# Performance work log

Measured on AMD Instinct MI355X. Metric: run time of the kernel, lower is better.

Reference implementation:

```python
import jax, jax.numpy as jnp
import numpy as np
from jax import lax


def conv2d(x, w, b, stride, pad):
    # x: NCHW, w: OIHW (PyTorch Conv2d layout)
    y = lax.conv_general_dilated(x, w, (stride, stride), ((pad, pad), (pad, pad)),
                                 dimension_numbers=('NCHW', 'OIHW', 'NCHW'))
    return y + b[None, :, None, None]


def conv_transpose2d(x, w, b, stride, pad):
    # PyTorch ConvTranspose2d weight layout: (in_ch, out_ch, kH, kW).
    # Equivalent to a conv with lhs dilation, flipped kernel, in/out swapped.
    k = w.shape[2]
    w2 = jnp.transpose(jnp.flip(w, (2, 3)), (1, 0, 2, 3))  # (out, in, k, k)
    p = k - 1 - pad
    y = lax.conv_general_dilated(x, w2, (1, 1), ((p, p), (p, p)),
                                 lhs_dilation=(stride, stride),
                                 dimension_numbers=('NCHW', 'OIHW', 'NCHW'))
    return y + b[None, :, None, None]


def setup_inputs() -> dict:
    key = jax.random.key(0)
    ks = jax.random.split(key, 8)
    K, D = 512, 64  # num_embeddings, embedding_dim
    x = jax.random.uniform(ks[0], (32, 3, 256, 256), jnp.float32)

    def he(k, shape, fan_in):
        return jax.random.normal(k, shape, jnp.float32) * np.float32(np.sqrt(2.0 / fan_in))

    w1 = he(ks[1], (64, 3, 4, 4), 3 * 16);   b1 = jnp.zeros((64,), jnp.float32)
    w2 = he(ks[2], (D, 64, 4, 4), 64 * 16);  b2 = jnp.zeros((D,), jnp.float32)
    # codebook init: uniform(-1/K, 1/K) as in the torch module
    codebook = jax.random.uniform(ks[3], (K, D), jnp.float32, -1.0 / K, 1.0 / K)
    dw1 = he(ks[4], (D, 64, 4, 4), D * 16);  db1 = jnp.zeros((64,), jnp.float32)
    dw2 = he(ks[5], (64, 3, 4, 4), 64 * 16); db2 = jnp.zeros((3,), jnp.float32)
    return dict(x=x, w1=w1, b1=b1, w2=w2, b2=b2, codebook=codebook,
                dw1=dw1, db1=db1, dw2=dw2, db2=db2)


def reference(x, w1, b1, w2, b2, codebook, dw1, db1, dw2, db2):
    # Encoder
    z_e = jax.nn.relu(conv2d(x, w1, b1, 2, 1))
    z_e = jax.nn.relu(conv2d(z_e, w2, b2, 2, 1))  # (N, D, H/4, W/4)
    D = z_e.shape[1]
    # Faithful to torch: .view(-1, C) on contiguous NCHW (NO channel permute)
    zf = z_e.reshape(-1, D)  # (N*Hq*Wq, D) given D == Hq here numerically; rows are contiguous slices
    # ||z - e||^2 = ||z||^2 + ||e||^2 - 2 z.e  -> (M, K) distance matrix
    d = (jnp.sum(zf * zf, axis=1, keepdims=True)
         + jnp.sum(codebook * codebook, axis=1)
         - 2.0 * (zf @ codebook.T))
    idx = jnp.argmin(d, axis=1)           # (M,) int
    z_q = codebook[idx].reshape(z_e.shape)  # gather + reshape back to z_e shape
    # Decoder
    h = jax.nn.relu(conv_transpose2d(z_q, dw1, db1, 2, 1))
    x_recon = jax.nn.sigmoid(conv_transpose2d(h, dw2, db2, 2, 1))
    return x_recon, z_q
```

## Files before the change

kernel.cpp:

```cpp
#include <hip/hip_runtime.h>
#include <math.h>


typedef __attribute__((ext_vector_type(8))) short short8;
typedef __attribute__((ext_vector_type(4))) short short4v;
typedef __attribute__((ext_vector_type(4))) float f32x4;

#define MFMA16(a, b, c) __builtin_amdgcn_mfma_f32_16x16x32_bf16((a), (b), (c), 0, 0, 0)

__device__ __forceinline__ short f2bf(float f) {
  union { float f; unsigned u; } x; x.f = f;
  unsigned r = (x.u + 0x7FFFu + ((x.u >> 16) & 1u)) >> 16;
  return (short)r;
}
__device__ __forceinline__ float bf2f(short s) {
  union { unsigned u; float f; } x;
  x.u = ((unsigned)(unsigned short)s) << 16;
  return x.f;
}

__global__ __launch_bounds__(256) void k_prep(const float* __restrict__ w2,
                                              const float* __restrict__ dw1,
                                              const float* __restrict__ dw2,
                                              const float* __restrict__ cb,
                                              short* __restrict__ A2,
                                              short* __restrict__ AD1,
                                              short* __restrict__ AD2,
                                              short* __restrict__ cbb,
                                              float* __restrict__ cnm) {
  int i = blockIdx.x * 256 + threadIdx.x;
  {
    int t = i >> 12, oc = (i >> 6) & 63, c = i & 63;
    A2[i] = f2bf(w2[(oc * 64 + c) * 16 + t]);
  }
  {
    int p = i >> 14, ab = (i >> 12) & 3, oc = (i >> 6) & 63, c = i & 63;
    int kh = 1 - (p >> 1) + 2 * (ab >> 1);
    int kw = 1 - (p & 1) + 2 * (ab & 1);
    AD1[i] = f2bf(dw1[(c * 64 + oc) * 16 + kh * 4 + kw]);
  }
  if (i < 16384) {
    int p = i >> 12, ab = (i >> 10) & 3, oc = (i >> 6) & 15, c = i & 63;
    int kh = 1 - (p >> 1) + 2 * (ab >> 1);
    int kw = 1 - (p & 1) + 2 * (ab & 1);
    short v = 0;
    if (oc < 3) v = f2bf(dw2[(c * 3 + oc) * 16 + kh * 4 + kw]);
    AD2[i] = v;
  }
  if (i < 32768) cbb[i] = f2bf(cb[i]);
  if (i < 512) {
    float s = 0.f;
    for (int d = 0; d < 64; ++d) { float v = cb[i * 64 + d]; s += v * v; }
    cnm[i] = s;
  }
}

__global__ __launch_bounds__(256) void k_conv1(const float* __restrict__ x,
                                               const float* __restrict__ w1,
                                               const float* __restrict__ b1,
                                               short* __restrict__ z1T) {
  __shared__ float sW[3 * 16 * 64];
  __shared__ float sB[64];
  __shared__ float sIn[3 * 34 * 34];
  __shared__ short sOutC[256 * 72];
  const int tid = threadIdx.x;

  {
    float tw[12];
#pragma unroll
    for (int it = 0; it < 12; ++it) {
      int i = tid + 256 * it;
      int oc = i & 63, t = (i >> 6) & 15, c = i >> 10;
      tw[it] = w1[(oc * 3 + c) * 16 + t];
    }
#pragma unroll
    for (int it = 0; it < 12; ++it) sW[tid + 256 * it] = tw[it];
  }
  if (tid < 64) sB[tid] = b1[tid];

  const int b = blockIdx.x;
  const int n = b >> 6;
  const int tile = b & 63;
  const int tr = tile >> 3, tc = tile & 7;
  const int oh0 = tr * 16, ow0 = tc * 16;
  const int ih_base = oh0 * 2 - 1, iw_base = ow0 * 2 - 1;

  {
    float t[14]; bool vd[14];
#pragma unroll
    for (int it = 0; it < 14; ++it) {
      int i = tid + 256 * it;
      vd[it] = i < 3468;
      int ii = vd[it] ? i : 0;
      int c = ii / 1156;
      int rem = ii - c * 1156;
      int r = rem / 34;
      int col = rem - r * 34;
      int ih = ih_base + r, iw = iw_base + col;
      float v = 0.f;
      if (vd[it] && (unsigned)ih < 256u && (unsigned)iw < 256u)
        v = x[((n * 3 + c) * 256 + ih) * 256 + iw];
      t[it] = v;
    }
#pragma unroll
    for (int it = 0; it < 14; ++it)
      if (vd[it]) sIn[tid + 256 * it] = t[it];
  }
  __syncthreads();

  const int ty = tid >> 4, tx = tid & 15;
  float acc[64];
#pragma unroll
  for (int j = 0; j < 64; ++j) acc[j] = sB[j];

  for (int c = 0; c < 3; ++c) {
    for (int t = 0; t < 16; ++t) {
      int kh = t >> 2, kw = t & 3;
      float v = sIn[c * 1156 + (2 * ty + kh) * 34 + (2 * tx + kw)];
      const float4* wp = (const float4*)&sW[(c * 16 + t) * 64];
#pragma unroll
      for (int j = 0; j < 16; ++j) {
        float4 w4 = wp[j];
        acc[4 * j + 0] += v * w4.x;
        acc[4 * j + 1] += v * w4.y;
        acc[4 * j + 2] += v * w4.z;
        acc[4 * j + 3] += v * w4.w;
      }
    }
  }

  const int sp = ty * 16 + tx;
#pragma unroll
  for (int kk = 0; kk < 8; ++kk) {
    short8 v;
#pragma unroll
    for (int t2 = 0; t2 < 8; ++t2) {
      float r = acc[8 * kk + t2];
      v[t2] = f2bf(r > 0.f ? r : 0.f);
    }
    *(short8*)&sOutC[sp * 72 + 8 * kk] = v;
  }
  __syncthreads();
  const int r = tid >> 4, jj = tid & 15;
#pragma unroll
  for (int it = 0; it < 8; ++it) {
    int chunk = jj + 16 * it;
    int owL = chunk >> 3, c8 = chunk & 7;
    short8 v = *(const short8*)&sOutC[(r * 16 + owL) * 72 + 8 * c8];
    *(short8*)(z1T + (((long)(n * 128 + oh0 + r) * 128) + ow0 + owL) * 64 + 8 * c8) = v;
  }
}

__global__ __launch_bounds__(256) void k_conv2(const short* __restrict__ z1T,
                                               const short* __restrict__ A2,
                                               const float* __restrict__ b2,
                                               short* __restrict__ ze) {
  __shared__ char smemC[62400];
  __shared__ float sB2c[64];
  short* slab = (short*)smemC;
  short* sOut = (short*)smemC;

  const int tid = threadIdx.x;
  if (tid < 64) sB2c[tid] = b2[tid];
  const int b = blockIdx.x;
  const int n = b >> 5;
  const int oh0 = (b & 31) * 2;
  const int w = tid >> 6, l = tid & 63;
  const int row = w >> 1, mh = w & 1;
  const int e = l & 15, kg = l >> 4;
  const int ih0 = 2 * oh0 - 1;

  f32x4 acc[2][4];
#pragma unroll
  for (int mi = 0; mi < 2; ++mi)
#pragma unroll
    for (int nt = 0; nt < 4; ++nt) acc[mi][nt] = (f32x4){0.f, 0.f, 0.f, 0.f};

  for (int p = 0; p < 2; ++p) {
    const int c0 = 32 * p;
    __syncthreads();
    {
      short8 ta[7]; int off[7];
#pragma unroll
      for (int it = 0; it < 7; ++it) {
        int i = tid + 256 * it;
        int r = i / 520;
        int rem = i - r * 520;
        int iwL = rem >> 2, li = rem & 3;
        int ih = ih0 + r, iw = iwL - 1;
        off[it] = 8 * ((r * 130 + iwL) * 5 + li);
        short8 v = {0, 0, 0, 0, 0, 0, 0, 0};
        if ((unsigned)ih < 128u && (unsigned)iw < 128u)
          v = *(const short8*)(z1T + (((long)(n * 128 + ih) * 128) + iw) * 64 + c0 + 8 * li);
        ta[it] = v;
      }
#pragma unroll
      for (int it = 0; it < 7; ++it) *(short8*)&slab[off[it]] = ta[it];
    }
    {
      short8 tb[6]; int off[6]; bool vd[6];
#pragma unroll
      for (int it = 0; it < 6; ++it) {
        int i = tid + 256 * (7 + it);
        vd[it] = i < 3120;
        int ii = vd[it] ? i : 0;
        int r = ii / 520;
        int rem = ii - r * 520;
        int iwL = rem >> 2, li = rem & 3;
        int ih = ih0 + r, iw = iwL - 1;
        off[it] = 8 * ((r * 130 + iwL) * 5 + li);
        short8 v = {0, 0, 0, 0, 0, 0, 0, 0};
        if (vd[it] && (unsigned)ih < 128u && (unsigned)iw < 128u)
          v = *(const short8*)(z1T + (((long)(n * 128 + ih) * 128) + iw) * 64 + c0 + 8 * li);
        tb[it] = v;
      }
#pragma unroll
      for (int it = 0; it < 6; ++it)
        if (vd[it]) *(short8*)&slab[off[it]] = tb[it];
    }
    __syncthreads();

    for (int t = 0; t < 16; ++t) {
      const int kh = t >> 2, kw = t & 3;
      const int rL = 2 * row + kh;
      short8 aF[2], bF[4];
#pragma unroll
      for (int mi = 0; mi < 2; ++mi)
        aF[mi] = *(const short8*)(A2 + ((t * 64 + 32 * mh + 16 * mi + e) * 64) + c0 + 8 * kg);
#pragma unroll
      for (int nt = 0; nt < 4; ++nt) {
        int iwL = 2 * (nt * 16 + e) + kw;
        bF[nt] = *(const short8*)&slab[8 * ((rL * 130 + iwL) * 5 + kg)];
      }
#pragma unroll
      for (int mi = 0; mi < 2; ++mi)
#pragma unroll
        for (int nt = 0; nt < 4; ++nt)
          acc[mi][nt] = MFMA16(aF[mi], bF[nt], acc[mi][nt]);
    }
  }

  __syncthreads();
#pragma unroll
  for (int mi = 0; mi < 2; ++mi)
#pragma unroll
    for (int nt = 0; nt < 4; ++nt)
#pragma unroll
      for (int rr = 0; rr < 4; ++rr) {
        int oc = 32 * mh + 16 * mi + 4 * kg + rr;
        float v = acc[mi][nt][rr] + sB2c[oc];
        sOut[(row * 64 + oc) * 68 + nt * 16 + e] = f2bf(v > 0.f ? v : 0.f);
      }
  __syncthreads();
  {
    int oc = 32 * mh + (l >> 1);
    int half = l & 1;
#pragma unroll
    for (int j = 0; j < 8; ++j) {
      short4v v = *(const short4v*)&sOut[(row * 64 + oc) * 68 + 32 * half + 4 * j];
      *(short4v*)(ze + (((long)(n * 64 + oc) * 64) + oh0 + row) * 64 + 32 * half + 4 * j) = v;
    }
  }
}

__global__ __launch_bounds__(256) void k_vq(const short* __restrict__ zeb,
                                            const short* __restrict__ cbb,
                                            const float* __restrict__ cnm,
                                            const float* __restrict__ cb,
                                            float* __restrict__ zq,
                                            short* __restrict__ zqT) {
  __shared__ short sT[64 * 68];
  const int tid = threadIdx.x;
  const int wv = tid >> 6, l = tid & 63;
  const int e = l & 15, kg = l >> 4;
  const int b = blockIdx.x;
  const int n = b >> 6, h = b & 63;

  const short* zebase = zeb + (((long)(n * 64 + 16 * wv + e) * 64) + h) * 64;
  short8 aF0 = *(const short8*)(zebase + 8 * kg);
  short8 aF1 = *(const short8*)(zebase + 32 + 8 * kg);

  float bestD[4];
  int bestI[4];
#pragma unroll
  for (int rr = 0; rr < 4; ++rr) { bestD[rr] = 3.4e38f; bestI[rr] = 0; }

  for (int ch = 0; ch < 8; ++ch) {
    f32x4 acc[4];
#pragma unroll
    for (int nt = 0; nt < 4; ++nt) {
      acc[nt] = (f32x4){0.f, 0.f, 0.f, 0.f};
      const short* cbase = cbb + (ch * 64 + nt * 16 + e) * 64;
      short8 b0 = *(const short8*)(cbase + 8 * kg);
      short8 b1 = *(const short8*)(cbase + 32 + 8 * kg);
      acc[nt] = MFMA16(aF0, b0, acc[nt]);
      acc[nt] = MFMA16(aF1, b1, acc[nt]);
    }
#pragma unroll
    for (int nt = 0; nt < 4; ++nt) {
      int code = ch * 64 + nt * 16 + e;
      float cn = cnm[code];
#pragma unroll
      for (int rr = 0; rr < 4; ++rr) {
        float d = cn - 2.f * acc[nt][rr];
        if (d < bestD[rr]) { bestD[rr] = d; bestI[rr] = code; }
      }
    }
  }
#pragma unroll
  for (int m = 1; m <= 8; m <<= 1) {
#pragma unroll
    for (int rr = 0; rr < 4; ++rr) {
      float od = __shfl_xor(bestD[rr], m);
      int oi = __shfl_xor(bestI[rr], m);
      if (od < bestD[rr] || (od == bestD[rr] && oi < bestI[rr])) {
        bestD[rr] = od; bestI[rr] = oi;
      }
    }
  }
#pragma unroll
  for (int rr = 0; rr < 4; ++rr) {
    int c = 16 * wv + 4 * kg + rr;
    int idx = bestI[rr];
    float4 v = *(const float4*)(cb + idx * 64 + 4 * e);
    *(float4*)(zq + (((long)(n * 64 + c) * 64) + h) * 64 + 4 * e) = v;
    sT[(4 * e + 0) * 68 + c] = f2bf(v.x);
    sT[(4 * e + 1) * 68 + c] = f2bf(v.y);
    sT[(4 * e + 2) * 68 + c] = f2bf(v.z);
    sT[(4 * e + 3) * 68 + c] = f2bf(v.w);
  }
  __syncthreads();
  {
    int wq = tid >> 2, hq = tid & 3;
    short8 v0 = *(const short8*)&sT[wq * 68 + 16 * hq];
    short8 v1 = *(const short8*)&sT[wq * 68 + 16 * hq + 8];
    short* dst = zqT + (((long)(n * 64 + h) * 64) + wq) * 64 + 16 * hq;
    *(short8*)dst = v0;
    *(short8*)(dst + 8) = v1;
  }
}

__global__ __launch_bounds__(256) void k_deconv1(const short* __restrict__ zqT,
                                                 const short* __restrict__ AD1,
                                                 const float* __restrict__ db1,
                                                 short* __restrict__ hT) {
  __shared__ char smemD[34816];
  __shared__ float sBias[64];
  short* slab = (short*)smemD;
  short* sOut = (short*)smemD;

  const int tid = threadIdx.x;
  if (tid < 64) sBias[tid] = db1[tid];
  const int b = blockIdx.x;
  const int n = b >> 6, i0 = b & 63;
  const int w = tid >> 6, l = tid & 63;
  const int ph = w >> 1, pw = w & 1;
  const int e = l & 15, kg = l >> 4;

  {
    short8 t[7]; int off[7]; bool vd[7];
#pragma unroll
    for (int it = 0; it < 7; ++it) {
      int i = tid + 256 * it;
      vd[it] = i < 1584;
      int ii = vd[it] ? i : 0;
      int r = ii / 528;
      int rem = ii - r * 528;
      int iwL = rem >> 3, li = rem & 7;
      int ih = i0 - 1 + r, iw = iwL - 1;
      off[it] = (r * 66 + iwL) * 72 + 8 * li;
      short8 v = {0, 0, 0, 0, 0, 0, 0, 0};
      if (vd[it] && (unsigned)ih < 64u && (unsigned)iw < 64u)
        v = *(const short8*)(zqT + (((long)(n * 64 + ih) * 64) + iw) * 64 + 8 * li);
      t[it] = v;
    }
#pragma unroll
    for (int it = 0; it < 7; ++it)
      if (vd[it]) *(short8*)&slab[off[it]] = t[it];
  }
  __syncthreads();

  f32x4 acc[4][4];
#pragma unroll
  for (int m = 0; m < 4; ++m)
#pragma unroll
    for (int nt = 0; nt < 4; ++nt) acc[m][nt] = (f32x4){0.f, 0.f, 0.f, 0.f};

  for (int ab = 0; ab < 4; ++ab) {
    const int rL = 1 + ph - (ab >> 1);
    const int coff = pw - (ab & 1) + 1;
#pragma unroll
    for (int ks = 0; ks < 2; ++ks) {
      short8 aF[4], bF[4];
#pragma unroll
      for (int m = 0; m < 4; ++m)
        aF[m] = *(const short8*)(AD1 + (((w * 4 + ab) * 64 + 16 * m + e) * 64) + 32 * ks + 8 * kg);
#pragma unroll
      for (int nt = 0; nt < 4; ++nt) {
        int iwL = nt * 16 + e + coff;
        bF[nt] = *(const short8*)&slab[(rL * 66 + iwL) * 72 + 32 * ks + 8 * kg];
      }
#pragma unroll
      for (int m = 0; m < 4; ++m)
#pragma unroll
        for (int nt = 0; nt < 4; ++nt)
          acc[m][nt] = MFMA16(aF[m], bF[nt], acc[m][nt]);
    }
  }

  __syncthreads();
#pragma unroll
  for (int m = 0; m < 4; ++m)
#pragma unroll
    for (int nt = 0; nt < 4; ++nt) {
      int owIdx = nt * 16 + e;
      int oc0 = 16 * m + 4 * kg;
      short4v o;
#pragma unroll
      for (int rr = 0; rr < 4; ++rr) {
        float v = acc[m][nt][rr] + sBias[oc0 + rr];
        o[rr] = f2bf(v > 0.f ? v : 0.f);
      }
      *(short4v*)&sOut[((w * 64 + owIdx) * 68) + oc0] = o;
    }
  __syncthreads();
  {
    const int oh = 2 * i0 + ph;
    const int ow = 2 * l + pw;
    short* dst = hT + (((long)(n * 128 + oh) * 128) + ow) * 64;
#pragma unroll
    for (int j = 0; j < 16; ++j) {
      short4v v = *(const short4v*)&sOut[((w * 64 + l) * 68) + 4 * j];
      *(short4v*)(dst + 4 * j) = v;
    }
  }
}

__global__ __launch_bounds__(512) void k_deconv2(const short* __restrict__ hT,
                                                 const short* __restrict__ AD2,
                                                 const float* __restrict__ db2,
                                                 float* __restrict__ xr) {
  __shared__ __align__(16) char smem[56160];
  __shared__ float sB2[3];
  short* slab = (short*)smem;
  float* sOut = (float*)smem;

  const int tid = threadIdx.x;
  if (tid < 3) sB2[tid] = db2[tid];
  const int b = blockIdx.x;
  const int n = b >> 5;
  const int band = b & 31;
  const int w = tid >> 6, l = tid & 63;
  const int ph = w >> 2, pw = (w >> 1) & 1, chf = w & 1;
  const int p = ph * 2 + pw;
  const int e = l & 15, kg = l >> 4;

  int soff[7]; long sga[7]; bool sv[7], sinb[7];
#pragma unroll
  for (int it = 0; it < 7; ++it) {
    int i = tid + 512 * it;
    sv[it] = i < 3120;
    int ii = sv[it] ? i : 0;
    int r = ii / 520;
    int rm = ii - r * 520;
    int iwL = rm >> 2, li = rm & 3;
    int ih = 4 * band - 1 + r, iw = iwL - 1;
    sinb[it] = sv[it] && (unsigned)ih < 128u && (unsigned)iw < 128u;
    soff[it] = (r * 130 + iwL) * 36 + 8 * li;
    sga[it] = (((long)(n * 128 + ih) * 128) + iw) * 64 + 8 * li;
  }

  {
    short8 t0[7];
#pragma unroll
    for (int it = 0; it < 7; ++it) {
      short8 v = {0, 0, 0, 0, 0, 0, 0, 0};
      if (sinb[it]) v = *(const short8*)(hT + sga[it]);
      t0[it] = v;
    }
#pragma unroll
    for (int it = 0; it < 7; ++it)
      if (sv[it]) *(short8*)&slab[soff[it]] = t0[it];
  }
  __syncthreads();

  short8 t1[7];
#pragma unroll
  for (int it = 0; it < 7; ++it) {
    short8 v = {0, 0, 0, 0, 0, 0, 0, 0};
    if (sinb[it]) v = *(const short8*)(hT + sga[it] + 32);
    t1[it] = v;
  }

  f32x4 acc[4][4];
#pragma unroll
  for (int j = 0; j < 4; ++j)
#pragma unroll
    for (int nt = 0; nt < 4; ++nt) acc[j][nt] = (f32x4){0.f, 0.f, 0.f, 0.f};

  const int colBase = 64 * chf + e + pw + 1;
  {
    short8 aF[4];
#pragma unroll
    for (int ab = 0; ab < 4; ++ab)
      aF[ab] = *(const short8*)(AD2 + (((p * 4 + ab) * 16 + e) * 64) + 8 * kg);
#pragma unroll
    for (int ab = 0; ab < 4; ++ab) {
      const int a = ab >> 1, bb = ab & 1;
#pragma unroll
      for (int j = 0; j < 4; ++j) {
        const int rL = j + ph - a + 1;
#pragma unroll
        for (int nt = 0; nt < 4; ++nt) {
          const int iwL = nt * 16 + colBase - bb;
          short8 bf = *(const short8*)&slab[(rL * 130 + iwL) * 36 + 8 * kg];
          acc[j][nt] = MFMA16(aF[ab], bf, acc[j][nt]);
        }
      }
    }
  }
  __syncthreads();

#pragma unroll
  for (int it = 0; it < 7; ++it)
    if (sv[it]) *(short8*)&slab[soff[it]] = t1[it];
  __syncthreads();
  {
    short8 aF[4];
#pragma unroll
    for (int ab = 0; ab < 4; ++ab)
      aF[ab] = *(const short8*)(AD2 + (((p * 4 + ab) * 16 + e) * 64) + 32 + 8 * kg);
#pragma unroll
    for (int ab = 0; ab < 4; ++ab) {
      const int a = ab >> 1, bb = ab & 1;
#pragma unroll
      for (int j = 0; j < 4; ++j) {
        const int rL = j + ph - a + 1;
#pragma unroll
        for (int nt = 0; nt < 4; ++nt) {
          const int iwL = nt * 16 + colBase - bb;
          short8 bf = *(const short8*)&slab[(rL * 130 + iwL) * 36 + 8 * kg];
          acc[j][nt] = MFMA16(aF[ab], bf, acc[j][nt]);
        }
      }
    }
  }
  __syncthreads();

  if (kg == 0) {
#pragma unroll
    for (int j = 0; j < 4; ++j)
#pragma unroll
      for (int nt = 0; nt < 4; ++nt) {
        int ohl = 2 * j + ph;
        int ow = 2 * (64 * chf + nt * 16 + e) + pw;
#pragma unroll
        for (int rr = 0; rr < 3; ++rr) {
          float v = 1.f / (1.f + expf(-(acc[j][nt][rr] + sB2[rr])));
          sOut[(rr * 8 + ohl) * 256 + ow] = v;
        }
      }
  }
  __syncthreads();
#pragma unroll
  for (int it = 0; it < 3; ++it) {
    int i = tid + 512 * it;
    int oc = i / 512, rem = i - oc * 512;
    int ohl = rem >> 6, c4 = rem & 63;
    float4 v = ((const float4*)sOut)[i];
    *(float4*)(xr + (((long)(n * 3 + oc) * 256) + 8 * band + ohl) * 256 + 4 * c4) = v;
  }
}

extern "C" void kernel_launch(void* const* d_in, const int* in_sizes, int n_in,
                              void* d_out, int out_size, void* d_ws, size_t ws_size,
                              hipStream_t stream) {
  (void)in_sizes; (void)n_in; (void)out_size; (void)ws_size;

  const float* x   = (const float*)d_in[0];
  const float* w1  = (const float*)d_in[1];
  const float* b1  = (const float*)d_in[2];
  const float* w2  = (const float*)d_in[3];
  const float* b2  = (const float*)d_in[4];
  const float* cb  = (const float*)d_in[5];
  const float* dw1 = (const float*)d_in[6];
  const float* db1 = (const float*)d_in[7];
  const float* dw2 = (const float*)d_in[8];
  const float* db2 = (const float*)d_in[9];

  char* wsb = (char*)d_ws;
  short* z1T = (short*)wsb;
  short* zeb = (short*)(wsb + 67108864);
  short* zqT = (short*)(wsb + 83886080);
  short* A2  = (short*)(wsb + 100663296);
  short* AD1 = (short*)(wsb + 100794368);
  short* cbb = (short*)(wsb + 100925440);
  float* cnm = (float*)(wsb + 100990976);
  short* AD2 = (short*)(wsb + 100993024);
  short* hT  = z1T;

  float* xr = (float*)d_out;
  float* zq = (float*)d_out + 6291456;

  k_prep<<<256, 256, 0, stream>>>(w2, dw1, dw2, cb, A2, AD1, AD2, cbb, cnm);
  k_conv1<<<2048, 256, 0, stream>>>(x, w1, b1, z1T);
  k_conv2<<<1024, 256, 0, stream>>>(z1T, A2, b2, zeb);
  k_vq<<<2048, 256, 0, stream>>>(zeb, cbb, cnm, cb, zq, zqT);
  k_deconv1<<<2048, 256, 0, stream>>>(zqT, AD1, db1, hT);
  k_deconv2<<<1024, 512, 0, stream>>>(hT, AD2, db2, xr);
}
```

Baseline: 471.6 us.

## Load deconv input fragments directly from global instead of staging LDS slabs

Both transposed-conv kernels stop staging the input halo into shared memory. Each wave now loads its MFMA B fragments straight from global memory into registers. In deconv2 those loads rotate through two row buffers, interleaved with the MFMAs, and the bias is read directly from global. This removes the LDS staging barriers and shrinks shared memory, which could raise occupancy, but overlapping windows are now fetched redundantly from global/L2 and register pressure goes up.

After: 477.8 us. About the same (+1.3%).

```diff
diff --git a/kernel.cpp b/kernel.cpp
--- a/kernel.cpp
+++ b/kernel.cpp
@@ -344,85 +344,76 @@
                                                  const short* __restrict__ AD1,
                                                  const float* __restrict__ db1,
                                                  short* __restrict__ hT) {
-  __shared__ char smemD[34816];
-  __shared__ float sBias[64];
-  short* slab = (short*)smemD;
-  short* sOut = (short*)smemD;
-
+  __shared__ short sOut[4 * 64 * 68];
   const int tid = threadIdx.x;
-  if (tid < 64) sBias[tid] = db1[tid];
   const int b = blockIdx.x;
   const int n = b >> 6, i0 = b & 63;
   const int w = tid >> 6, l = tid & 63;
   const int ph = w >> 1, pw = w & 1;
   const int e = l & 15, kg = l >> 4;
 
-  {
-    short8 t[7]; int off[7]; bool vd[7];
-#pragma unroll
-    for (int it = 0; it < 7; ++it) {
-      int i = tid + 256 * it;
-      vd[it] = i < 1584;
-      int ii = vd[it] ? i : 0;
-      int r = ii / 528;
-      int rem = ii - r * 528;
-      int iwL = rem >> 3, li = rem & 7;
-      int ih = i0 - 1 + r, iw = iwL - 1;
-      off[it] = (r * 66 + iwL) * 72 + 8 * li;
-      short8 v = {0, 0, 0, 0, 0, 0, 0, 0};
-      if (vd[it] && (unsigned)ih < 64u && (unsigned)iw < 64u)
-        v = *(const short8*)(zqT + (((long)(n * 64 + ih) * 64) + iw) * 64 + 8 * li);
-      t[it] = v;
-    }
-#pragma unroll
-    for (int it = 0; it < 7; ++it)
-      if (vd[it]) *(short8*)&slab[off[it]] = t[it];
-  }
-  __syncthreads();
-
   f32x4 acc[4][4];
 #pragma unroll
   for (int m = 0; m < 4; ++m)
 #pragma unroll
     for (int nt = 0; nt < 4; ++nt) acc[m][nt] = (f32x4){0.f, 0.f, 0.f, 0.f};
 
-  for (int ab = 0; ab < 4; ++ab) {
-    const int rL = 1 + ph - (ab >> 1);
-    const int coff = pw - (ab & 1) + 1;
-#pragma unroll
-    for (int ks = 0; ks < 2; ++ks) {
-      short8 aF[4], bF[4];
-#pragma unroll
-      for (int m = 0; m < 4; ++m)
-        aF[m] = *(const short8*)(AD1 + (((w * 4 + ab) * 64 + 16 * m + e) * 64) + 32 * ks + 8 * kg);
+#pragma unroll
+  for (int a = 0; a < 2; ++a) {
+    const int ih = i0 + ph - a;
+    const bool rowOk = (unsigned)ih < 64u;
+    const short* rowp = zqT + ((long)(n * 64 + ih) * 64) * 64 + 8 * kg;
+
+    short8 Bf[2][2][4];
+#pragma unroll
+    for (int bb = 0; bb < 2; ++bb)
 #pragma unroll
       for (int nt = 0; nt < 4; ++nt) {
-        int iwL = nt * 16 + e + coff;
-        bF[nt] = *(const short8*)&slab[(rL * 66 + iwL) * 72 + 32 * ks + 8 * kg];
-      }
-#pragma unroll
-      for (int m = 0; m < 4; ++m)
-#pragma unroll
-        for (int nt = 0; nt < 4; ++nt)
-          acc[m][nt] = MFMA16(aF[m], bF[nt], acc[m][nt]);
-    }
-  }
-
-  __syncthreads();
-#pragma unroll
-  for (int m = 0; m < 4; ++m)
+        const int iw = nt * 16 + e + pw - bb;
+        const bool v = rowOk && ((unsigned)iw < 64u);
+#pragma unroll
+        for (int ks = 0; ks < 2; ++ks) {
+          short8 t = {0, 0, 0, 0, 0, 0, 0, 0};
+          if (v) t = *(const short8*)(rowp + (long)iw * 64 + 32 * ks);
+          Bf[bb][ks][nt] = t;
+        }
+      }
+
+#pragma unroll
+    for (int bb = 0; bb < 2; ++bb) {
+      const int ab = 2 * a + bb;
+#pragma unroll
+      for (int ks = 0; ks < 2; ++ks) {
+        short8 aF[4];
+#pragma unroll
+        for (int m = 0; m < 4; ++m)
+          aF[m] = *(const short8*)(AD1 + (((w * 4 + ab) * 64 + 16 * m + e) * 64) + 32 * ks + 8 * kg);
+#pragma unroll
+        for (int m = 0; m < 4; ++m)
+#pragma unroll
+          for (int nt = 0; nt < 4; ++nt)
+            acc[m][nt] = MFMA16(aF[m], Bf[bb][ks][nt], acc[m][nt]);
+      }
+    }
+  }
+
+#pragma unroll
+  for (int m = 0; m < 4; ++m) {
+    const int oc0 = 16 * m + 4 * kg;
+    const float4 bv = *(const float4*)(db1 + oc0);
+    const float bvv[4] = {bv.x, bv.y, bv.z, bv.w};
 #pragma unroll
     for (int nt = 0; nt < 4; ++nt) {
       int owIdx = nt * 16 + e;
-      int oc0 = 16 * m + 4 * kg;
       short4v o;
 #pragma unroll
       for (int rr = 0; rr < 4; ++rr) {
-        float v = acc[m][nt][rr] + sBias[oc0 + rr];
+        float v = acc[m][nt][rr] + bvv[rr];
         o[rr] = f2bf(v > 0.f ? v : 0.f);
       }
       *(short4v*)&sOut[((w * 64 + owIdx) * 68) + oc0] = o;
     }
+  }
   __syncthreads();
   {
     const int oh = 2 * i0 + ph;
@@ -440,13 +431,8 @@
                                                  const short* __restrict__ AD2,
                                                  const float* __restrict__ db2,
                                                  float* __restrict__ xr) {
-  __shared__ __align__(16) char smem[56160];
-  __shared__ float sB2[3];
-  short* slab = (short*)smem;
-  float* sOut = (float*)smem;
-
+  __shared__ float sOut[3 * 8 * 256];
   const int tid = threadIdx.x;
-  if (tid < 3) sB2[tid] = db2[tid];
   const int b = blockIdx.x;
   const int n = b >> 5;
   const int band = b & 31;
@@ -454,43 +440,7 @@
   const int ph = w >> 2, pw = (w >> 1) & 1, chf = w & 1;
   const int p = ph * 2 + pw;
   const int e = l & 15, kg = l >> 4;
-
-  int soff[7]; long sga[7]; bool sv[7], sinb[7];
-#pragma unroll
-  for (int it = 0; it < 7; ++it) {
-    int i = tid + 512 * it;
-    sv[it] = i < 3120;
-    int ii = sv[it] ? i : 0;
-    int r = ii / 520;
-    int rm = ii - r * 520;
-    int iwL = rm >> 2, li = rm & 3;
-    int ih = 4 * band - 1 + r, iw = iwL - 1;
-    sinb[it] = sv[it] && (unsigned)ih < 128u && (unsigned)iw < 128u;
-    soff[it] = (r * 130 + iwL) * 36 + 8 * li;
-    sga[it] = (((long)(n * 128 + ih) * 128) + iw) * 64 + 8 * li;
-  }
-
-  {
-    short8 t0[7];
-#pragma unroll
-    for (int it = 0; it < 7; ++it) {
-      short8 v = {0, 0, 0, 0, 0, 0, 0, 0};
-      if (sinb[it]) v = *(const short8*)(hT + sga[it]);
-      t0[it] = v;
-    }
-#pragma unroll
-    for (int it = 0; it < 7; ++it)
-      if (sv[it]) *(short8*)&slab[soff[it]] = t0[it];
-  }
-  __syncthreads();
-
-  short8 t1[7];
-#pragma unroll
-  for (int it = 0; it < 7; ++it) {
-    short8 v = {0, 0, 0, 0, 0, 0, 0, 0};
-    if (sinb[it]) v = *(const short8*)(hT + sga[it] + 32);
-    t1[it] = v;
-  }
+  const int colb = 64 * chf + e + pw;
 
   f32x4 acc[4][4];
 #pragma unroll
@@ -498,56 +448,58 @@
 #pragma unroll
     for (int nt = 0; nt < 4; ++nt) acc[j][nt] = (f32x4){0.f, 0.f, 0.f, 0.f};
 
-  const int colBase = 64 * chf + e + pw + 1;
-  {
+#define D2_LOADROW(R, rr_)                                                     \
+  {                                                                            \
+    const int rg_ = (rr_);                                                     \
+    short8 z_ = {0, 0, 0, 0, 0, 0, 0, 0};                                      \
+    if ((unsigned)rg_ < 128u) {                                                \
+      const short* rp_ = hT + ((long)(n * 128 + rg_) * 128) * 64 +             \
+                         32 * chh + 8 * kg;                                    \
+      _Pragma("unroll") for (int bb_ = 0; bb_ < 2; ++bb_)                      \
+          _Pragma("unroll") for (int nt_ = 0; nt_ < 4; ++nt_) {                \
+        const int iw_ = colb + nt_ * 16 - bb_;                                 \
+        short8 t_ = z_;                                                        \
+        if ((unsigned)iw_ < 128u) t_ = *(const short8*)(rp_ + (long)iw_ * 64); \
+        R[bb_][nt_] = t_;                                                      \
+      }                                                                        \
+    } else {                                                                   \
+      _Pragma("unroll") for (int bb_ = 0; bb_ < 2; ++bb_)                      \
+          _Pragma("unroll") for (int nt_ = 0; nt_ < 4; ++nt_) R[bb_][nt_] = z_;\
+    }                                                                          \
+  }
+
+#define D2_MM(jj_, aa_, R)                                                     \
+  {                                                                            \
+    _Pragma("unroll") for (int bb_ = 0; bb_ < 2; ++bb_) {                      \
+      const short8 af_ = aF[2 * (aa_) + bb_];                                  \
+      _Pragma("unroll") for (int nt_ = 0; nt_ < 4; ++nt_)                      \
+          acc[jj_][nt_] = MFMA16(af_, R[bb_][nt_], acc[jj_][nt_]);             \
+    }                                                                          \
+  }
+
+#pragma unroll
+  for (int chh = 0; chh < 2; ++chh) {
     short8 aF[4];
 #pragma unroll
     for (int ab = 0; ab < 4; ++ab)
-      aF[ab] = *(const short8*)(AD2 + (((p * 4 + ab) * 16 + e) * 64) + 8 * kg);
-#pragma unroll
-    for (int ab = 0; ab < 4; ++ab) {
-      const int a = ab >> 1, bb = ab & 1;
-#pragma unroll
-      for (int j = 0; j < 4; ++j) {
-        const int rL = j + ph - a + 1;
-#pragma unroll
-        for (int nt = 0; nt < 4; ++nt) {
-          const int iwL = nt * 16 + colBase - bb;
-          short8 bf = *(const short8*)&slab[(rL * 130 + iwL) * 36 + 8 * kg];
-          acc[j][nt] = MFMA16(aF[ab], bf, acc[j][nt]);
-        }
-      }
-    }
-  }
-  __syncthreads();
-
-#pragma unroll
-  for (int it = 0; it < 7; ++it)
-    if (sv[it]) *(short8*)&slab[soff[it]] = t1[it];
-  __syncthreads();
-  {
-    short8 aF[4];
-#pragma unroll
-    for (int ab = 0; ab < 4; ++ab)
-      aF[ab] = *(const short8*)(AD2 + (((p * 4 + ab) * 16 + e) * 64) + 32 + 8 * kg);
-#pragma unroll
-    for (int ab = 0; ab < 4; ++ab) {
-      const int a = ab >> 1, bb = ab & 1;
-#pragma unroll
-      for (int j = 0; j < 4; ++j) {
-        const int rL = j + ph - a + 1;
-#pragma unroll
-        for (int nt = 0; nt < 4; ++nt) {
-          const int iwL = nt * 16 + colBase - bb;
-          short8 bf = *(const short8*)&slab[(rL * 130 + iwL) * 36 + 8 * kg];
-          acc[j][nt] = MFMA16(aF[ab], bf, acc[j][nt]);
-        }
-      }
-    }
-  }
-  __syncthreads();
+      aF[ab] = *(const short8*)(AD2 + (((p * 4 + ab) * 16 + e) * 64) + 32 * chh + 8 * kg);
+
+    short8 R0[2][4], R1[2][4];
+    const int rbase = 4 * band + ph - 1;
+    D2_LOADROW(R0, rbase + 0)
+    D2_LOADROW(R1, rbase + 1)
+
+    D2_MM(0, 1, R0) D2_LOADROW(R0, rbase + 2) D2_MM(0, 0, R1)
+    D2_MM(1, 1, R1) D2_LOADROW(R1, rbase + 3) D2_MM(1, 0, R0)
+    D2_MM(2, 1, R0) D2_LOADROW(R0, rbase + 4) D2_MM(2, 0, R1)
+    D2_MM(3, 1, R1)                           D2_MM(3, 0, R0)
+  }
+#undef D2_LOADROW
+#undef D2_MM
 
   if (kg == 0) {
+    const float b0 = db2[0], b1v = db2[1], b2v = db2[2];
+    const float bias3[3] = {b0, b1v, b2v};
 #pragma unroll
     for (int j = 0; j < 4; ++j)
 #pragma unroll
@@ -556,7 +508,7 @@
         int ow = 2 * (64 * chf + nt * 16 + e) + pw;
 #pragma unroll
         for (int rr = 0; rr < 3; ++rr) {
-          float v = 1.f / (1.f + expf(-(acc[j][nt][rr] + sB2[rr])));
+          float v = 1.f / (1.f + expf(-(acc[j][nt][rr] + bias3[rr])));
           sOut[(rr * 8 + ohl) * 256 + ow] = v;
         }
       }
```
